# Optimization experiments

Measured on AMD Instinct MI355X. Metric: run time of the kernel, lower is better.

Reference implementation:

```python
import jax, jax.numpy as jnp
import numpy as np

DIM = 2048
NUM_HEADS = 16
HEAD_DIM = DIM // NUM_HEADS  # 128
HIDDEN = HEAD_DIM * NUM_HEADS  # 2048


def setup_inputs() -> dict:
    key = jax.random.key(0)
    k1, k2, k3 = jax.random.split(key, 3)
    x = jax.random.normal(k1, (2, 4096, DIM), dtype=jnp.float32)
    # match torch init: gates.weight ~ N(0, dim**-0.5), output.weight ~ N(0, hidden**-0.5)
    Wg = jax.random.normal(k2, (NUM_HEADS + 3 * HIDDEN, DIM), dtype=jnp.float32) * DIM ** -0.5
    bg = jnp.zeros((NUM_HEADS + 3 * HIDDEN,), dtype=jnp.float32)
    Wo = jax.random.normal(k3, (DIM, HIDDEN), dtype=jnp.float32) * HIDDEN ** -0.5
    bo = jnp.zeros((DIM,), dtype=jnp.float32)
    return {"x": x, "Wg": Wg, "bg": bg, "Wo": Wo, "bo": bo}


def _combine(a, b):
    # linear recurrence c_t = f_t * c_{t-1} + u_t as an associative op
    fa, ua = a
    fb, ub = b
    return fa * fb, fb * ua + ub


def reference(x, Wg, bg, Wo, bo):
    # x: [B, T, dim]
    g = jnp.einsum('btd,gd->btg', x, Wg) + bg  # [B, T, H + 3*hidden]
    f = jax.nn.sigmoid(g[..., :NUM_HEADS])  # [B, T, H]
    i = jax.nn.sigmoid(g[..., NUM_HEADS:NUM_HEADS + HIDDEN])
    t = jnp.tanh(g[..., NUM_HEADS + HIDDEN:NUM_HEADS + 2 * HIDDEN])
    o = g[..., NUM_HEADS + 2 * HIDDEN:]
    f = jnp.repeat(f, HEAD_DIM, axis=-1)  # tied forget gate per head -> [B, T, hidden]
    update = i * t
    # scan over time axis (axis=1)
    _, c = jax.lax.associative_scan(_combine, (f, update), axis=1)
    h = o * jnp.tanh(c)
    return jnp.einsum('bth,dh->btd', h, Wo) + bo
```

## Files before the change

kernel.cpp:

```cpp
#include <hip/hip_runtime.h>
#include <hip/hip_bf16.h>

#define DIM 2048
#define NHEADS 16
#define HEAD_DIM 128
#define HIDDEN 2048
#define SEQ 4096
#define BATCH 2
#define BT (BATCH * SEQ)
#define NSEG 64
#define SEGLEN (SEQ / NSEG)
#define N_GATE (3 * HIDDEN)

typedef __bf16 bf16_t;
typedef __bf16 bf16x8 __attribute__((ext_vector_type(8)));
typedef __bf16 bf16x4_t __attribute__((ext_vector_type(4)));
typedef float f32x4 __attribute__((ext_vector_type(4)));

__device__ __forceinline__ void gload_lds16(const void* g, void* l) {
  __builtin_amdgcn_global_load_lds(
      (const __attribute__((address_space(1))) void*)g,
      (__attribute__((address_space(3))) void*)l, 16, 0, 0);
}

__global__ void cvt_f32_bf16(const float* __restrict__ src, bf16_t* __restrict__ dst, int n4) {
  int i = blockIdx.x * blockDim.x + threadIdx.x;
  if (i >= n4) return;
  float4 v = reinterpret_cast<const float4*>(src)[i];
  bf16x4_t o;
  o[0] = (bf16_t)v.x; o[1] = (bf16_t)v.y; o[2] = (bf16_t)v.z; o[3] = (bf16_t)v.w;
  reinterpret_cast<bf16x4_t*>(dst)[i] = o;
}

__global__ void fgate_kernel(const float* __restrict__ x, const float* __restrict__ Wg,
                             const float* __restrict__ bg, float* __restrict__ fout) {
  int idx = blockIdx.x * 256 + threadIdx.x;
  int bt = idx >> 4, h = idx & 15;
  const float* xr = x + (size_t)bt * DIM;
  const float* wr = Wg + (size_t)h * DIM;
  float acc = 0.f;
  for (int k = 0; k < DIM; k += 4) {
    float4 xv = *reinterpret_cast<const float4*>(xr + k);
    float4 wv = *reinterpret_cast<const float4*>(wr + k);
    acc = fmaf(xv.x, wv.x, acc);
    acc = fmaf(xv.y, wv.y, acc);
    acc = fmaf(xv.z, wv.z, acc);
    acc = fmaf(xv.w, wv.w, acc);
  }
  acc += bg[h];
  fout[idx] = 1.f / (1.f + expf(-acc));
}

template <int MODE>
__global__ void gemm_bt(const bf16_t* __restrict__ A, const bf16_t* __restrict__ B,
                        const float* __restrict__ bias,
                        bf16_t* __restrict__ Oi, bf16_t* __restrict__ Ot,
                        bf16_t* __restrict__ Oo, float* __restrict__ Of,
                        int K) {
  __shared__ __align__(16) bf16_t As[128 * 32];
  __shared__ __align__(16) bf16_t Bs[128 * 32];
  const int tid = threadIdx.x;
  const int wave = tid >> 6, lane = tid & 63;
  const int brow = blockIdx.y * 128, bcol = blockIdx.x * 128;
  const int wm = wave >> 1, wn = wave & 1;

  f32x4 acc[4][4] = {};

  const int ldrow = lane >> 2;
  const int ldcol = (lane & 3) * 8;

  for (int k0 = 0; k0 < K; k0 += 32) {
#pragma unroll
    for (int j = 0; j < 2; ++j) {
      int rg = wave * 2 + j;
      int row = rg * 16 + ldrow;
      gload_lds16(A + (size_t)(brow + row) * K + k0 + ldcol, &As[rg * 16 * 32]);
      gload_lds16(B + (size_t)(bcol + row) * K + k0 + ldcol, &Bs[rg * 16 * 32]);
    }
    __syncthreads();

    bf16x8 af[4], bfr[4];
#pragma unroll
    for (int mi = 0; mi < 4; ++mi)
      af[mi] = *reinterpret_cast<const bf16x8*>(
          &As[(wm * 64 + mi * 16 + (lane & 15)) * 32 + (lane >> 4) * 8]);
#pragma unroll
    for (int ni = 0; ni < 4; ++ni)
      bfr[ni] = *reinterpret_cast<const bf16x8*>(
          &Bs[(wn * 64 + ni * 16 + (lane & 15)) * 32 + (lane >> 4) * 8]);
#pragma unroll
    for (int mi = 0; mi < 4; ++mi)
#pragma unroll
      for (int ni = 0; ni < 4; ++ni)
        acc[mi][ni] = __builtin_amdgcn_mfma_f32_16x16x32_bf16(af[mi], bfr[ni], acc[mi][ni], 0, 0, 0);
    __syncthreads();
  }

  const int crow0 = brow + wm * 64;
  const int ccol0 = bcol + wn * 64;
  if (MODE == 0) {
    const int section = bcol >> 11;
    bf16_t* dst = (section == 0) ? Oi : ((section == 1) ? Ot : Oo);
#pragma unroll
    for (int mi = 0; mi < 4; ++mi)
#pragma unroll
      for (int ni = 0; ni < 4; ++ni) {
        int gcol = ccol0 + ni * 16 + (lane & 15);
        int col = gcol & 2047;
        float b = bias[gcol];
#pragma unroll
        for (int q = 0; q < 4; ++q) {
          int row = crow0 + mi * 16 + (lane >> 4) * 4 + q;
          float v = acc[mi][ni][q] + b;
          float a;
          if (section == 0)      a = 1.f / (1.f + __expf(-v));
          else if (section == 1) a = tanhf(v);
          else                   a = v;
          dst[(size_t)row * HIDDEN + col] = (bf16_t)a;
        }
      }
  } else {
#pragma unroll
    for (int mi = 0; mi < 4; ++mi)
#pragma unroll
      for (int ni = 0; ni < 4; ++ni) {
        int col = ccol0 + ni * 16 + (lane & 15);
        float b = bias[col];
#pragma unroll
        for (int q = 0; q < 4; ++q) {
          int row = crow0 + mi * 16 + (lane >> 4) * 4 + q;
          Of[(size_t)row * DIM + col] = acc[mi][ni][q] + b;
        }
      }
  }
}

__global__ void scan_pass1(const float* __restrict__ fg, const bf16_t* __restrict__ gi,
                           const bf16_t* __restrict__ gt, float* __restrict__ cend,
                           float* __restrict__ pseg) {
  int bx = blockIdx.x;
  int chblk = bx & 7, seg = (bx >> 3) & 63, b = bx >> 9;
  int ch = chblk * 256 + threadIdx.x;
  int head = ch >> 7;
  float c = 0.f, P = 1.f;
  size_t t0 = (size_t)b * SEQ + (size_t)seg * SEGLEN;
  for (int tt = 0; tt < SEGLEN; ++tt) {
    size_t bt = t0 + tt;
    float f = fg[bt * NHEADS + head];
    float iv = (float)gi[bt * HIDDEN + ch];
    float tv = (float)gt[bt * HIDDEN + ch];
    c = fmaf(f, c, iv * tv);
    P *= f;
  }
  size_t o = ((size_t)b * NSEG + seg) * HIDDEN + ch;
  cend[o] = c;
  pseg[o] = P;
}

__global__ void scan_pass2(const float* __restrict__ cend, const float* __restrict__ pseg,
                           float* __restrict__ cin) {
  int idx = blockIdx.x * 256 + threadIdx.x;
  int b = idx >> 11, ch = idx & 2047;
  float C = 0.f;
  for (int s = 0; s < NSEG; ++s) {
    size_t o = ((size_t)b * NSEG + s) * HIDDEN + ch;
    cin[o] = C;
    C = cend[o] + pseg[o] * C;
  }
}

__global__ void scan_pass3(const float* __restrict__ fg, const bf16_t* __restrict__ gi,
                           const bf16_t* __restrict__ gt, const bf16_t* __restrict__ go,
                           const float* __restrict__ cin, bf16_t* __restrict__ h) {
  int bx = blockIdx.x;
  int chblk = bx & 7, seg = (bx >> 3) & 63, b = bx >> 9;
  int ch = chblk * 256 + threadIdx.x;
  int head = ch >> 7;
  float c = cin[((size_t)b * NSEG + seg) * HIDDEN + ch];
  size_t t0 = (size_t)b * SEQ + (size_t)seg * SEGLEN;
  for (int tt = 0; tt < SEGLEN; ++tt) {
    size_t bt = t0 + tt;
    float f = fg[bt * NHEADS + head];
    float iv = (float)gi[bt * HIDDEN + ch];
    float tv = (float)gt[bt * HIDDEN + ch];
    c = fmaf(f, c, iv * tv);
    float hv = (float)go[bt * HIDDEN + ch] * tanhf(c);
    h[bt * HIDDEN + ch] = (bf16_t)hv;
  }
}

extern "C" void kernel_launch(void* const* d_in, const int* in_sizes, int n_in,
                              void* d_out, int out_size, void* d_ws, size_t ws_size,
                              hipStream_t stream) {
  const float* x  = (const float*)d_in[0];
  const float* Wg = (const float*)d_in[1];
  const float* bg = (const float*)d_in[2];
  const float* Wo = (const float*)d_in[3];
  const float* bo = (const float*)d_in[4];
  float* out = (float*)d_out;

  char* ws = (char*)d_ws;
  size_t off = 0;
  auto alloc = [&](size_t bytes) -> void* {
    void* p = ws + off;
    off += (bytes + 255) & ~(size_t)255;
    return p;
  };
  bf16_t* xb   = (bf16_t*)alloc((size_t)BT * DIM * 2);
  bf16_t* wgb  = (bf16_t*)alloc((size_t)N_GATE * DIM * 2);
  bf16_t* wob  = (bf16_t*)alloc((size_t)DIM * HIDDEN * 2);
  float*  fg   = (float*)alloc((size_t)BT * NHEADS * 4);
  bf16_t* gi   = (bf16_t*)alloc((size_t)BT * HIDDEN * 2);
  bf16_t* gt   = (bf16_t*)alloc((size_t)BT * HIDDEN * 2);
  bf16_t* go   = (bf16_t*)alloc((size_t)BT * HIDDEN * 2);
  bf16_t* hbuf = (bf16_t*)alloc((size_t)BT * HIDDEN * 2);
  float*  cend = (float*)alloc((size_t)BATCH * NSEG * HIDDEN * 4);
  float*  pseg = (float*)alloc((size_t)BATCH * NSEG * HIDDEN * 4);
  float*  cin  = (float*)alloc((size_t)BATCH * NSEG * HIDDEN * 4);
  (void)ws_size; (void)in_sizes; (void)n_in; (void)out_size;

  {
    int n4 = BT * DIM / 4;
    cvt_f32_bf16<<<(n4 + 255) / 256, 256, 0, stream>>>(x, xb, n4);
  }
  {
    int n4 = N_GATE * DIM / 4;
    cvt_f32_bf16<<<(n4 + 255) / 256, 256, 0, stream>>>(Wg + (size_t)NHEADS * DIM, wgb, n4);
  }
  {
    int n4 = DIM * HIDDEN / 4;
    cvt_f32_bf16<<<(n4 + 255) / 256, 256, 0, stream>>>(Wo, wob, n4);
  }

  fgate_kernel<<<(BT * NHEADS) / 256, 256, 0, stream>>>(x, Wg, bg, fg);

  gemm_bt<0><<<dim3(N_GATE / 128, BT / 128), 256, 0, stream>>>(
      xb, wgb, bg + NHEADS, gi, gt, go, nullptr, DIM);

  scan_pass1<<<BATCH * NSEG * (HIDDEN / 256), 256, 0, stream>>>(fg, gi, gt, cend, pseg);
  scan_pass2<<<BATCH * HIDDEN / 256, 256, 0, stream>>>(cend, pseg, cin);
  scan_pass3<<<BATCH * NSEG * (HIDDEN / 256), 256, 0, stream>>>(fg, gi, gt, go, cin, hbuf);

  gemm_bt<1><<<dim3(DIM / 128, BT / 128), 256, 0, stream>>>(
      hbuf, wob, bo, nullptr, nullptr, nullptr, out, HIDDEN);
}
```

Measured before the change: 563.5 us.

## Replace GEMM with 256x256 tiled, 4-stage pipelined, LDS-swizzled MFMA kernel

Replaces the 128x128 single-buffered bf16 GEMM with a 256x256-tile, 512-thread kernel that keeps a 4-deep ring of LDS buffers. Async global-to-LDS loads are issued three k-steps ahead and paced with explicit vmcnt waits, so memory latency overlaps the MFMA work. It also XOR-swizzles the LDS layout to avoid bank conflicts, remaps block IDs for L2 locality, and raises MFMA priority with setprio. The cost is a hardcoded K of 2048, heavy register pressure from 32 accumulators per lane, and one block per CU.

```diff
diff --git a/kernel.cpp b/kernel.cpp
--- a/kernel.cpp
+++ b/kernel.cpp
@@ -51,58 +51,100 @@
   fout[idx] = 1.f / (1.f + expf(-acc));
 }
 
+
+__device__ __forceinline__ void stage_one(const bf16_t* __restrict__ G, bf16_t* lds_op,
+                                          int grow0, int k0, int j, int wid, int lane) {
+  const int chunk = j * 512 + wid * 64 + lane;
+  const int row = chunk >> 2;
+  const int c4s = chunk & 3;
+  const int c4d = c4s ^ (row & 3);
+  const bf16_t* src = G + (size_t)(grow0 + row) * 2048 + k0 + c4d * 8;
+  bf16_t* dst = lds_op + (j * 512 + wid * 64) * 8;
+  gload_lds16(src, dst);
+}
+
 template <int MODE>
-__global__ void gemm_bt(const bf16_t* __restrict__ A, const bf16_t* __restrict__ B,
-                        const float* __restrict__ bias,
-                        bf16_t* __restrict__ Oi, bf16_t* __restrict__ Ot,
-                        bf16_t* __restrict__ Oo, float* __restrict__ Of,
-                        int K) {
-  __shared__ __align__(16) bf16_t As[128 * 32];
-  __shared__ __align__(16) bf16_t Bs[128 * 32];
+__global__ __launch_bounds__(512, 1)
+void gemm256(const bf16_t* __restrict__ A, const bf16_t* __restrict__ B,
+             const float* __restrict__ bias,
+             bf16_t* __restrict__ Oi, bf16_t* __restrict__ Ot, bf16_t* __restrict__ Oo,
+             float* __restrict__ Of, int tiles_n) {
+  __shared__ __align__(16) bf16_t As[4][256 * 32];
+  __shared__ __align__(16) bf16_t Bs[4][256 * 32];
+  constexpr int KT = 64;
+
   const int tid = threadIdx.x;
-  const int wave = tid >> 6, lane = tid & 63;
-  const int brow = blockIdx.y * 128, bcol = blockIdx.x * 128;
-  const int wm = wave >> 1, wn = wave & 1;
-
-  f32x4 acc[4][4] = {};
-
-  const int ldrow = lane >> 2;
-  const int ldcol = (lane & 3) * 8;
-
-  for (int k0 = 0; k0 < K; k0 += 32) {
+  const int wid = tid >> 6, lane = tid & 63;
+  const int nwg = gridDim.x;
+  const int bid = blockIdx.x;
+  const int swz = (bid & 7) * (nwg >> 3) + (bid >> 3);
+  const int tm = swz / tiles_n;
+  const int tn = swz - tm * tiles_n;
+  const int brow = tm * 256, bcol = tn * 256;
+  const int wm = wid >> 2, wn = wid & 3;
+
+  f32x4 acc[8][4] = {};
+
+#pragma unroll
+  for (int t = 0; t < 3; ++t) {
 #pragma unroll
     for (int j = 0; j < 2; ++j) {
-      int rg = wave * 2 + j;
-      int row = rg * 16 + ldrow;
-      gload_lds16(A + (size_t)(brow + row) * K + k0 + ldcol, &As[rg * 16 * 32]);
-      gload_lds16(B + (size_t)(bcol + row) * K + k0 + ldcol, &Bs[rg * 16 * 32]);
+      stage_one(A, As[t], brow, t * 32, j, wid, lane);
+      stage_one(B, Bs[t], bcol, t * 32, j, wid, lane);
     }
-    __syncthreads();
-
-    bf16x8 af[4], bfr[4];
-#pragma unroll
-    for (int mi = 0; mi < 4; ++mi)
-      af[mi] = *reinterpret_cast<const bf16x8*>(
-          &As[(wm * 64 + mi * 16 + (lane & 15)) * 32 + (lane >> 4) * 8]);
-#pragma unroll
-    for (int ni = 0; ni < 4; ++ni)
-      bfr[ni] = *reinterpret_cast<const bf16x8*>(
-          &Bs[(wn * 64 + ni * 16 + (lane & 15)) * 32 + (lane >> 4) * 8]);
-#pragma unroll
-    for (int mi = 0; mi < 4; ++mi)
-#pragma unroll
-      for (int ni = 0; ni < 4; ++ni)
-        acc[mi][ni] = __builtin_amdgcn_mfma_f32_16x16x32_bf16(af[mi], bfr[ni], acc[mi][ni], 0, 0, 0);
-    __syncthreads();
-  }
-
-  const int crow0 = brow + wm * 64;
+  }
+
+  for (int kt = 0; kt < KT; ++kt) {
+    if (kt < KT - 2)       asm volatile("s_waitcnt vmcnt(8)" ::: "memory");
+    else if (kt == KT - 2) asm volatile("s_waitcnt vmcnt(4)" ::: "memory");
+    else                   asm volatile("s_waitcnt vmcnt(0)" ::: "memory");
+    __builtin_amdgcn_s_barrier();
+    asm volatile("" ::: "memory");
+
+    const int s = kt & 3;
+    const bf16_t* as = As[s];
+    const bf16_t* bs = Bs[s];
+    const bool do_stage = (kt + 3) < KT;
+    const int s3 = (kt + 3) & 3;
+    const int k03 = (kt + 3) * 32;
+
+    bf16x8 bfr[4];
+#pragma unroll
+    for (int ni = 0; ni < 4; ++ni) {
+      int r = wn * 64 + ni * 16 + (lane & 15);
+      bfr[ni] = *reinterpret_cast<const bf16x8*>(&bs[r * 32 + (((lane >> 4) ^ (r & 3))) * 8]);
+    }
+
+#pragma unroll
+    for (int q = 0; q < 4; ++q) {
+      if (do_stage) {
+        if (q < 2) stage_one(A, As[s3], brow, k03, q, wid, lane);
+        else       stage_one(B, Bs[s3], bcol, k03, q - 2, wid, lane);
+      }
+      int r0 = wm * 128 + (2 * q) * 16 + (lane & 15);
+      int r1 = r0 + 16;
+      bf16x8 af0 = *reinterpret_cast<const bf16x8*>(&as[r0 * 32 + (((lane >> 4) ^ (r0 & 3))) * 8]);
+      bf16x8 af1 = *reinterpret_cast<const bf16x8*>(&as[r1 * 32 + (((lane >> 4) ^ (r1 & 3))) * 8]);
+      __builtin_amdgcn_s_setprio(1);
+#pragma unroll
+      for (int ni = 0; ni < 4; ++ni) {
+        acc[2 * q][ni]     = __builtin_amdgcn_mfma_f32_16x16x32_bf16(af0, bfr[ni], acc[2 * q][ni], 0, 0, 0);
+        acc[2 * q + 1][ni] = __builtin_amdgcn_mfma_f32_16x16x32_bf16(af1, bfr[ni], acc[2 * q + 1][ni], 0, 0, 0);
+      }
+      __builtin_amdgcn_s_setprio(0);
+    }
+    asm volatile("" ::: "memory");
+    __builtin_amdgcn_s_barrier();
+    asm volatile("" ::: "memory");
+  }
+
+  const int crow0 = brow + wm * 128;
   const int ccol0 = bcol + wn * 64;
   if (MODE == 0) {
     const int section = bcol >> 11;
     bf16_t* dst = (section == 0) ? Oi : ((section == 1) ? Ot : Oo);
 #pragma unroll
-    for (int mi = 0; mi < 4; ++mi)
+    for (int mi = 0; mi < 8; ++mi)
 #pragma unroll
       for (int ni = 0; ni < 4; ++ni) {
         int gcol = ccol0 + ni * 16 + (lane & 15);
@@ -121,7 +163,7 @@
       }
   } else {
 #pragma unroll
-    for (int mi = 0; mi < 4; ++mi)
+    for (int mi = 0; mi < 8; ++mi)
 #pragma unroll
       for (int ni = 0; ni < 4; ++ni) {
         int col = ccol0 + ni * 16 + (lane & 15);
@@ -234,13 +276,11 @@
 
   fgate_kernel<<<(BT * NHEADS) / 256, 256, 0, stream>>>(x, Wg, bg, fg);
 
-  gemm_bt<0><<<dim3(N_GATE / 128, BT / 128), 256, 0, stream>>>(
-      xb, wgb, bg + NHEADS, gi, gt, go, nullptr, DIM);
+  gemm256<0><<<768, 512, 0, stream>>>(xb, wgb, bg + NHEADS, gi, gt, go, nullptr, 24);
 
   scan_pass1<<<BATCH * NSEG * (HIDDEN / 256), 256, 0, stream>>>(fg, gi, gt, cend, pseg);
   scan_pass2<<<BATCH * HIDDEN / 256, 256, 0, stream>>>(cend, pseg, cin);
   scan_pass3<<<BATCH * NSEG * (HIDDEN / 256), 256, 0, stream>>>(fg, gi, gt, go, cin, hbuf);
 
-  gemm_bt<1><<<dim3(DIM / 128, BT / 128), 256, 0, stream>>>(
-      hbuf, wob, bo, nullptr, nullptr, nullptr, out, HIDDEN);
-}
+  gemm256<1><<<256, 512, 0, stream>>>(hbuf, wob, bo, nullptr, nullptr, nullptr, out, 8);
+}
```

Measured after the change: 656.4 us. 16.5% more time.

## Replace GEMM with 256x256 tiled, double-buffered, swizzled MFMA pipeline

Applied to the files above, without the earlier changes.

Replaces the simple 128x128 single-buffer GEMM with a 256x256-tile, 8-wave kernel that double-buffers K-chunks in LDS, issues async global-to-LDS loads interleaved with MFMA phases, uses an XOR swizzle on LDS columns to avoid bank conflicts, and remaps block IDs for L2 locality. The aim is to hide global load latency behind compute and raise arithmetic intensity per tile. It uses more LDS and registers (one block per CU) and hand-tuned waitcnt and barrier ordering, which must be exactly right to be correct.

```diff
diff --git a/kernel.cpp b/kernel.cpp
--- a/kernel.cpp
+++ b/kernel.cpp
@@ -22,6 +22,12 @@
       (const __attribute__((address_space(1))) void*)g,
       (__attribute__((address_space(3))) void*)l, 16, 0, 0);
 }
+
+#define MEMFENCE asm volatile("" ::: "memory")
+#define BAR do { MEMFENCE; __builtin_amdgcn_s_barrier(); MEMFENCE; } while (0)
+#define LGKM0 do { asm volatile("s_waitcnt lgkmcnt(0)" ::: "memory"); \
+                   __builtin_amdgcn_sched_barrier(0); } while (0)
+#define VMCNT(n) asm volatile("s_waitcnt vmcnt(" #n ")" ::: "memory")
 
 __global__ void cvt_f32_bf16(const float* __restrict__ src, bf16_t* __restrict__ dst, int n4) {
   int i = blockIdx.x * blockDim.x + threadIdx.x;
@@ -51,67 +57,146 @@
   fout[idx] = 1.f / (1.f + expf(-acc));
 }
 
+
+__device__ __forceinline__ void stage_unit(const bf16_t* __restrict__ G, int grow0, int gcol,
+                                           bf16_t* region, int rh, int wid, int lane) {
+  const int r = rh * 128 + wid * 16 + (lane >> 2);
+  const int c = (lane & 3) ^ ((lane >> 2) & 3);
+  gload_lds16(G + (size_t)(grow0 + r) * 2048 + gcol + c * 8,
+              region + (rh * 128 + wid * 16) * 32);
+}
+
 template <int MODE>
-__global__ void gemm_bt(const bf16_t* __restrict__ A, const bf16_t* __restrict__ B,
-                        const float* __restrict__ bias,
-                        bf16_t* __restrict__ Oi, bf16_t* __restrict__ Ot,
-                        bf16_t* __restrict__ Oo, float* __restrict__ Of,
-                        int K) {
-  __shared__ __align__(16) bf16_t As[128 * 32];
-  __shared__ __align__(16) bf16_t Bs[128 * 32];
+__global__ __launch_bounds__(512, 1)
+void gemm256(const bf16_t* __restrict__ A, const bf16_t* __restrict__ B,
+             const float* __restrict__ bias,
+             bf16_t* __restrict__ Oi, bf16_t* __restrict__ Ot, bf16_t* __restrict__ Oo,
+             float* __restrict__ Of, int tiles_n) {
+  __shared__ __align__(16) bf16_t As[2][2][256 * 32];
+  __shared__ __align__(16) bf16_t Bs[2][2][256 * 32];
+  constexpr int KT = 32;
+
   const int tid = threadIdx.x;
-  const int wave = tid >> 6, lane = tid & 63;
-  const int brow = blockIdx.y * 128, bcol = blockIdx.x * 128;
-  const int wm = wave >> 1, wn = wave & 1;
-
-  f32x4 acc[4][4] = {};
-
-  const int ldrow = lane >> 2;
-  const int ldcol = (lane & 3) * 8;
-
-  for (int k0 = 0; k0 < K; k0 += 32) {
-#pragma unroll
-    for (int j = 0; j < 2; ++j) {
-      int rg = wave * 2 + j;
-      int row = rg * 16 + ldrow;
-      gload_lds16(A + (size_t)(brow + row) * K + k0 + ldcol, &As[rg * 16 * 32]);
-      gload_lds16(B + (size_t)(bcol + row) * K + k0 + ldcol, &Bs[rg * 16 * 32]);
-    }
-    __syncthreads();
-
-    bf16x8 af[4], bfr[4];
+  const int wid = tid >> 6, lane = tid & 63;
+  const int nwg = gridDim.x, bid = blockIdx.x;
+  const int swz = (bid & 7) * (nwg >> 3) + (bid >> 3);
+  const int tm = swz / tiles_n, tn = swz - tm * tiles_n;
+  const int brow = tm * 256, bcol = tn * 256;
+  const int wm = wid >> 2, wn = wid & 3;
+  const int rl = lane & 15, q = lane >> 4;
+  const int fo = (q ^ (rl & 3)) << 3;
+  const int arow0 = wm * 128 + rl;
+  const int brow0 = wn * 64 + rl;
+
+  f32x4 acc[8][4] = {};
+
+#define FRAG(regptr, row) (*reinterpret_cast<const bf16x8*>(&(regptr)[(row) * 32 + fo]))
+
+#pragma unroll
+  for (int rh = 0; rh < 2; ++rh) stage_unit(A, brow, 0,      &As[0][0][0], rh, wid, lane);
+#pragma unroll
+  for (int rh = 0; rh < 2; ++rh) stage_unit(B, bcol, 0,      &Bs[0][0][0], rh, wid, lane);
+#pragma unroll
+  for (int rh = 0; rh < 2; ++rh) stage_unit(A, brow, 32,     &As[0][1][0], rh, wid, lane);
+#pragma unroll
+  for (int rh = 0; rh < 2; ++rh) stage_unit(B, bcol, 32,     &Bs[0][1][0], rh, wid, lane);
+#pragma unroll
+  for (int rh = 0; rh < 2; ++rh) stage_unit(A, brow, 64,     &As[1][0][0], rh, wid, lane);
+#pragma unroll
+  for (int rh = 0; rh < 2; ++rh) stage_unit(B, bcol, 64,     &Bs[1][0][0], rh, wid, lane);
+  VMCNT(8);
+  BAR;
+
+  for (int t = 0; t < KT; ++t) {
+    const int slot = t & 1, nslot = slot ^ 1;
+    const bool s1 = (t + 1) < KT, s2 = (t + 2) < KT;
+    const int kc1 = (t + 1) * 64, kc2 = (t + 2) * 64;
+    const bf16_t* a0 = &As[slot][0][0];
+    const bf16_t* a1 = &As[slot][1][0];
+    const bf16_t* b0 = &Bs[slot][0][0];
+    const bf16_t* b1 = &Bs[slot][1][0];
+    bf16x8 bf[4], af[4];
+
+#pragma unroll
+    for (int ni = 0; ni < 4; ++ni) bf[ni] = FRAG(b0, brow0 + ni * 16);
+#pragma unroll
+    for (int mi = 0; mi < 4; ++mi) af[mi] = FRAG(a0, arow0 + mi * 16);
+    if (s1) { stage_unit(A, brow, kc1 + 32, &As[nslot][1][0], 0, wid, lane);
+              stage_unit(A, brow, kc1 + 32, &As[nslot][1][0], 1, wid, lane); }
+    BAR; LGKM0;
+    __builtin_amdgcn_s_setprio(1);
 #pragma unroll
     for (int mi = 0; mi < 4; ++mi)
-      af[mi] = *reinterpret_cast<const bf16x8*>(
-          &As[(wm * 64 + mi * 16 + (lane & 15)) * 32 + (lane >> 4) * 8]);
-#pragma unroll
-    for (int ni = 0; ni < 4; ++ni)
-      bfr[ni] = *reinterpret_cast<const bf16x8*>(
-          &Bs[(wn * 64 + ni * 16 + (lane & 15)) * 32 + (lane >> 4) * 8]);
+#pragma unroll
+      for (int ni = 0; ni < 4; ++ni)
+        acc[mi][ni] = __builtin_amdgcn_mfma_f32_16x16x32_bf16(af[mi], bf[ni], acc[mi][ni], 0, 0, 0);
+    __builtin_amdgcn_s_setprio(0);
+    BAR;
+
+#pragma unroll
+    for (int mi = 0; mi < 4; ++mi) af[mi] = FRAG(a0, arow0 + 64 + mi * 16);
+    if (s1) { stage_unit(B, bcol, kc1 + 32, &Bs[nslot][1][0], 0, wid, lane);
+              stage_unit(B, bcol, kc1 + 32, &Bs[nslot][1][0], 1, wid, lane); }
+    BAR; LGKM0;
+    __builtin_amdgcn_s_setprio(1);
 #pragma unroll
     for (int mi = 0; mi < 4; ++mi)
 #pragma unroll
       for (int ni = 0; ni < 4; ++ni)
-        acc[mi][ni] = __builtin_amdgcn_mfma_f32_16x16x32_bf16(af[mi], bfr[ni], acc[mi][ni], 0, 0, 0);
-    __syncthreads();
-  }
-
-  const int crow0 = brow + wm * 64;
+        acc[4 + mi][ni] = __builtin_amdgcn_mfma_f32_16x16x32_bf16(af[mi], bf[ni], acc[4 + mi][ni], 0, 0, 0);
+    __builtin_amdgcn_s_setprio(0);
+    if (t < KT - 1) { VMCNT(8); } else { VMCNT(0); }
+    BAR;
+
+#pragma unroll
+    for (int ni = 0; ni < 4; ++ni) bf[ni] = FRAG(b1, brow0 + ni * 16);
+#pragma unroll
+    for (int mi = 0; mi < 4; ++mi) af[mi] = FRAG(a1, arow0 + mi * 16);
+    if (s2) { stage_unit(A, brow, kc2, &As[slot][0][0], 0, wid, lane);
+              stage_unit(A, brow, kc2, &As[slot][0][0], 1, wid, lane); }
+    BAR; LGKM0;
+    __builtin_amdgcn_s_setprio(1);
+#pragma unroll
+    for (int mi = 0; mi < 4; ++mi)
+#pragma unroll
+      for (int ni = 0; ni < 4; ++ni)
+        acc[mi][ni] = __builtin_amdgcn_mfma_f32_16x16x32_bf16(af[mi], bf[ni], acc[mi][ni], 0, 0, 0);
+    __builtin_amdgcn_s_setprio(0);
+    BAR;
+
+#pragma unroll
+    for (int mi = 0; mi < 4; ++mi) af[mi] = FRAG(a1, arow0 + 64 + mi * 16);
+    if (s2) { stage_unit(B, bcol, kc2, &Bs[slot][0][0], 0, wid, lane);
+              stage_unit(B, bcol, kc2, &Bs[slot][0][0], 1, wid, lane); }
+    BAR; LGKM0;
+    __builtin_amdgcn_s_setprio(1);
+#pragma unroll
+    for (int mi = 0; mi < 4; ++mi)
+#pragma unroll
+      for (int ni = 0; ni < 4; ++ni)
+        acc[4 + mi][ni] = __builtin_amdgcn_mfma_f32_16x16x32_bf16(af[mi], bf[ni], acc[4 + mi][ni], 0, 0, 0);
+    __builtin_amdgcn_s_setprio(0);
+    if (t < KT - 2) { VMCNT(8); } else if (t == KT - 2) { VMCNT(4); } else { VMCNT(0); }
+    BAR;
+  }
+#undef FRAG
+
+  const int crow0 = brow + wm * 128;
   const int ccol0 = bcol + wn * 64;
   if (MODE == 0) {
     const int section = bcol >> 11;
     bf16_t* dst = (section == 0) ? Oi : ((section == 1) ? Ot : Oo);
 #pragma unroll
-    for (int mi = 0; mi < 4; ++mi)
+    for (int mi = 0; mi < 8; ++mi)
 #pragma unroll
       for (int ni = 0; ni < 4; ++ni) {
         int gcol = ccol0 + ni * 16 + (lane & 15);
         int col = gcol & 2047;
         float b = bias[gcol];
 #pragma unroll
-        for (int q = 0; q < 4; ++q) {
-          int row = crow0 + mi * 16 + (lane >> 4) * 4 + q;
-          float v = acc[mi][ni][q] + b;
+        for (int qq = 0; qq < 4; ++qq) {
+          int row = crow0 + mi * 16 + (lane >> 4) * 4 + qq;
+          float v = acc[mi][ni][qq] + b;
           float a;
           if (section == 0)      a = 1.f / (1.f + __expf(-v));
           else if (section == 1) a = tanhf(v);
@@ -121,15 +206,15 @@
       }
   } else {
 #pragma unroll
-    for (int mi = 0; mi < 4; ++mi)
+    for (int mi = 0; mi < 8; ++mi)
 #pragma unroll
       for (int ni = 0; ni < 4; ++ni) {
         int col = ccol0 + ni * 16 + (lane & 15);
         float b = bias[col];
 #pragma unroll
-        for (int q = 0; q < 4; ++q) {
-          int row = crow0 + mi * 16 + (lane >> 4) * 4 + q;
-          Of[(size_t)row * DIM + col] = acc[mi][ni][q] + b;
+        for (int qq = 0; qq < 4; ++qq) {
+          int row = crow0 + mi * 16 + (lane >> 4) * 4 + qq;
+          Of[(size_t)row * DIM + col] = acc[mi][ni][qq] + b;
         }
       }
   }
@@ -234,13 +319,11 @@
 
   fgate_kernel<<<(BT * NHEADS) / 256, 256, 0, stream>>>(x, Wg, bg, fg);
 
-  gemm_bt<0><<<dim3(N_GATE / 128, BT / 128), 256, 0, stream>>>(
-      xb, wgb, bg + NHEADS, gi, gt, go, nullptr, DIM);
+  gemm256<0><<<768, 512, 0, stream>>>(xb, wgb, bg + NHEADS, gi, gt, go, nullptr, 24);
 
   scan_pass1<<<BATCH * NSEG * (HIDDEN / 256), 256, 0, stream>>>(fg, gi, gt, cend, pseg);
   scan_pass2<<<BATCH * HIDDEN / 256, 256, 0, stream>>>(cend, pseg, cin);
   scan_pass3<<<BATCH * NSEG * (HIDDEN / 256), 256, 0, stream>>>(fg, gi, gt, go, cin, hbuf);
 
-  gemm_bt<1><<<dim3(DIM / 128, BT / 128), 256, 0, stream>>>(
-      hbuf, wob, bo, nullptr, nullptr, nullptr, out, HIDDEN);
-}
+  gemm256<1><<<256, 512, 0, stream>>>(hbuf, wob, bo, nullptr, nullptr, nullptr, out, 8);
+}
```

Measured after the change: 599.3 us. +6.4%, slower.
